# Kernel optimization log

Measured on AMD Instinct MI355X. Metric: run time of the kernel, lower is better.

Reference implementation:

```python
import jax, jax.numpy as jnp
import numpy as np

# Config (matches init_kwargs)
N, P, K, DIMS = 16, 1024, 16, 3
C_IN, C_MID, C_OUT, DM = 64, 64, 128, 4
C_CAT = C_MID + C_IN          # channels entering depthwise-separable conv
KK = K * K
BN_EPS = 1e-5


def setup_inputs() -> dict:
    key = jax.random.key(0)
    ks = jax.random.split(key, 24)
    s = 0.05  # small init scale for weights
    inp = {
        # forward args
        "rep_pt": jax.random.normal(ks[0], (N, P, DIMS), jnp.float32),
        "pts":    jax.random.normal(ks[1], (N, P, K, DIMS), jnp.float32),
        "fts":    jax.random.normal(ks[2], (N, P, K, C_IN), jnp.float32),
        # dense1 / dense2 (point lifting MLP), weights stored (in, out)
        "w1": jax.random.normal(ks[3], (DIMS, C_MID), jnp.float32) * s,
        "b1": jnp.zeros((C_MID,), jnp.float32),
        "w2": jax.random.normal(ks[4], (C_MID, C_MID), jnp.float32) * s,
        "b2": jnp.zeros((C_MID,), jnp.float32),
        # conv1: Conv2d(dims, K*K, (1,K)); weight (KK, dims, K)
        "wc1": jax.random.normal(ks[5], (KK, DIMS, K), jnp.float32) * s,
        "bc1": jnp.zeros((KK,), jnp.float32),
        # x_dense1 (ELU) and x_dense2 (no activation)
        "wx1": jax.random.normal(ks[6], (KK, KK), jnp.float32) * s,
        "bx1": jnp.zeros((KK,), jnp.float32),
        "wx2": jax.random.normal(ks[7], (KK, KK), jnp.float32) * s,
        "bx2": jnp.zeros((KK,), jnp.float32),
        # depthwise Conv2d(C_CAT, C_CAT*DM, (1,K), groups=C_CAT): weight (C_CAT, DM, K)
        "wdw": jax.random.normal(ks[8], (C_CAT, DM, K), jnp.float32) * s,
        "bdw": jnp.zeros((C_CAT * DM,), jnp.float32),
        # pointwise Conv2d(C_CAT*DM, C_OUT, 1): weight stored (C_CAT*DM, C_OUT)
        "wpw": jax.random.normal(ks[9], (C_CAT * DM, C_OUT), jnp.float32) * s,
        "bpw": jnp.zeros((C_OUT,), jnp.float32),
        # BatchNorm2d(C_OUT) in eval mode (running stats)
        "bn_gamma": jnp.ones((C_OUT,), jnp.float32),
        "bn_beta":  jnp.zeros((C_OUT,), jnp.float32),
        "bn_mean":  jax.random.normal(ks[10], (C_OUT,), jnp.float32) * 0.1,
        "bn_var":   jax.random.uniform(ks[11], (C_OUT,), jnp.float32, 0.5, 1.5),
    }
    return inp


def reference(rep_pt, pts, fts, w1, b1, w2, b2, wc1, bc1, wx1, bx1, wx2, bx2,
              wdw, bdw, wpw, bpw, bn_gamma, bn_beta, bn_mean, bn_var):
    elu = jax.nn.elu
    n, p, k = pts.shape[0], pts.shape[1], pts.shape[2]

    # localize points around representative point: (N,P,K,dims)
    pts_local = pts - rep_pt[:, :, None, :]

    # lift coordinates to C_mid features (two Dense+ELU)
    h = elu(pts_local @ w1 + b1)
    h = elu(h @ w2 + b2)
    fts_cat = jnp.concatenate([h, fts], axis=-1)  # (N,P,K,C_CAT)

    # learned X-transform: conv1 over the K neighbors -> (N,P,K*K)
    X = elu(jnp.einsum('npkd,odk->npo', pts_local, wc1) + bc1)
    X = elu(X @ wx1 + bx1)
    X = X @ wx2 + bx2            # x_dense2: no activation
    X = X.reshape(n, p, k, k)    # (N,P,K,K)

    # apply X-transform to concatenated features
    fts_X = jnp.einsum('npij,npjc->npic', X, fts_cat)  # (N,P,K,C_CAT)

    # depthwise conv (kernel (1,K), groups=C_CAT, depth multiplier DM)
    # torch grouped-conv channel order: out channel o = c*DM + d
    dw = jnp.einsum('npkc,cdk->npcd', fts_X, wdw).reshape(n, p, -1) + bdw
    # pointwise 1x1 conv -> C_OUT, then ELU
    y = elu(dw @ wpw + bpw)      # (N,P,C_OUT)
    # BatchNorm2d in eval mode (per-channel affine with running stats)
    y = (y - bn_mean) * (bn_gamma / jnp.sqrt(bn_var + BN_EPS)) + bn_beta
    return y                     # (N,P,C_OUT)
```

## Files before the change

kernel.cpp:

```cpp
#include <hip/hip_runtime.h>

#define NPTS 16384
#define MPB  16
#define NTHR 256
#define WS_NEEDED 401408u

typedef __attribute__((ext_vector_type(8))) short bf16x8;
typedef __attribute__((ext_vector_type(4))) float f32x4;

__device__ __forceinline__ unsigned short f2bf(float x) {
    unsigned u = __float_as_uint(x);
    return (unsigned short)((u + 0x7FFFu + ((u >> 16) & 1u)) >> 16);
}
__device__ __forceinline__ float bf2f(unsigned short h) {
    return __uint_as_float(((unsigned)h) << 16);
}
__device__ __forceinline__ float elu_f(float x) {
    return x > 0.f ? x : (__expf(x) - 1.f);
}

__device__ __forceinline__ bf16x8 load_bfrag(const float* __restrict__ W, int N,
                                             int kt, int nt, int lane) {
    int k0  = kt * 32 + ((lane >> 4) << 3);
    int col = nt * 16 + (lane & 15);
    const float* s = W + k0 * N + col;
    bf16x8 r;
#pragma unroll
    for (int j = 0; j < 8; j++) r[j] = (short)f2bf(s[j * N]);
    return r;
}

__global__ void pack_weights(const float* __restrict__ w2,
                             const float* __restrict__ wx1,
                             const float* __restrict__ wx2,
                             const float* __restrict__ wpw,
                             unsigned short* __restrict__ dst) {
    int gid  = blockIdx.x * 256 + threadIdx.x;
    int frag = gid >> 6, lane = gid & 63;
    const float* src; int N, fl;
    if      (frag <   8) { src = w2;  N =  64; fl = frag;       }
    else if (frag < 136) { src = wx1; N = 256; fl = frag - 8;   }
    else if (frag < 264) { src = wx2; N = 256; fl = frag - 136; }
    else                 { src = wpw; N = 128; fl = frag - 264; }
    int NT  = N >> 4;
    int kt  = fl / NT, nt = fl - kt * NT;
    int k0  = kt * 32 + (lane >> 4) * 8;
    int col = nt * 16 + (lane & 15);
    const float* s = src + k0 * N + col;
    unsigned v[4];
#pragma unroll
    for (int u = 0; u < 4; u++) {
        unsigned lo = f2bf(s[(2 * u) * N]);
        unsigned hi = f2bf(s[(2 * u + 1) * N]);
        v[u] = lo | (hi << 16);
    }
    *(uint4*)&dst[gid * 8] = make_uint4(v[0], v[1], v[2], v[3]);
}

template <bool PACKED>
__global__ __launch_bounds__(NTHR, 2)
void xconv_main(const float* __restrict__ rep_pt, const float* __restrict__ pts,
                const float* __restrict__ fts,
                const float* __restrict__ w1,  const float* __restrict__ b1,
                const float* __restrict__ w2,  const float* __restrict__ b2,
                const float* __restrict__ wc1, const float* __restrict__ bc1,
                const float* __restrict__ wx1, const float* __restrict__ bx1,
                const float* __restrict__ wx2, const float* __restrict__ bx2,
                const float* __restrict__ wdw, const float* __restrict__ bdw,
                const float* __restrict__ wpw, const float* __restrict__ bpw,
                const float* __restrict__ bn_gamma, const float* __restrict__ bn_beta,
                const float* __restrict__ bn_mean,  const float* __restrict__ bn_var,
                const unsigned short* __restrict__ wpack,
                float* __restrict__ out) {
    __shared__ __align__(16) char smem[62720];
    float*          s_ptsl = (float*)smem;
    unsigned short* s_h2   = (unsigned short*)(smem + 3072);
    unsigned short* s_h1   = (unsigned short*)(smem + 35840);
    unsigned short* s_x0   = (unsigned short*)(smem + 35840);
    unsigned short* s_x1   = (unsigned short*)(smem + 44288);
    unsigned short* s_dw   = (unsigned short*)(smem + 35840);
    unsigned short* s_x2   = (unsigned short*)(smem + 54272);

    const int t    = threadIdx.x;
    const int lane = t & 63;
    const int w    = t >> 6;
    const int gp0  = blockIdx.x * MPB;

    for (int idx = t; idx < MPB * 48; idx += NTHR) {
        int m = idx / 48, r = idx - m * 48;
        int k = r / 3,    d = r - k * 3;
        int gp = gp0 + m;
        s_ptsl[idx] = pts[(gp * 16 + k) * 3 + d] - rep_pt[gp * 3 + d];
    }
    __syncthreads();

    for (int R = 0; R < 2; R++) {
        {
            int lr  = t >> 1;
            int row = 128 * R + lr;
            int m = row >> 4, k = row & 15;
            float p0 = s_ptsl[m * 48 + k * 3 + 0];
            float p1 = s_ptsl[m * 48 + k * 3 + 1];
            float p2 = s_ptsl[m * 48 + k * 3 + 2];
            int cb = (t & 1) * 32;
#pragma unroll
            for (int cc = 0; cc < 4; cc++) {
                unsigned v[4];
#pragma unroll
                for (int u = 0; u < 4; u++) {
                    int c0 = cb + cc * 8 + u * 2;
                    float a  = fmaf(p0, w1[c0],       fmaf(p1, w1[64 + c0],     fmaf(p2, w1[128 + c0],     b1[c0])));
                    float bb = fmaf(p0, w1[c0 + 1],   fmaf(p1, w1[64 + c0 + 1], fmaf(p2, w1[128 + c0 + 1], b1[c0 + 1])));
                    v[u] = (unsigned)f2bf(elu_f(a)) | ((unsigned)f2bf(elu_f(bb)) << 16);
                }
                *(uint4*)&s_h1[lr * 72 + cb + cc * 8] = make_uint4(v[0], v[1], v[2], v[3]);
            }
        }
        __syncthreads();
        {
            const bf16x8* wp = (const bf16x8*)wpack;
            bf16x8 Bf[8];
#pragma unroll
            for (int f = 0; f < 8; f++) {
                if (PACKED) Bf[f] = wp[f * 64 + lane];
                else        Bf[f] = load_bfrag(w2, 64, f >> 2, f & 3, lane);
            }
            float bias[4];
#pragma unroll
            for (int nt = 0; nt < 4; nt++) bias[nt] = b2[nt * 16 + (lane & 15)];
#pragma unroll
            for (int i = 0; i < 2; i++) {
                int rtl = w * 2 + i;
                int g0  = (8 * R + rtl) * 16;
                bf16x8 a0 = *(const bf16x8*)&s_h1[(rtl * 16 + (lane & 15)) * 72 + 0  + (lane >> 4) * 8];
                bf16x8 a1 = *(const bf16x8*)&s_h1[(rtl * 16 + (lane & 15)) * 72 + 32 + (lane >> 4) * 8];
#pragma unroll
                for (int nt = 0; nt < 4; nt++) {
                    f32x4 acc = {bias[nt], bias[nt], bias[nt], bias[nt]};
                    acc = __builtin_amdgcn_mfma_f32_16x16x32_bf16(a0, Bf[0 * 4 + nt], acc, 0, 0, 0);
                    acc = __builtin_amdgcn_mfma_f32_16x16x32_bf16(a1, Bf[1 * 4 + nt], acc, 0, 0, 0);
#pragma unroll
                    for (int r = 0; r < 4; r++) {
                        int krow = (lane >> 4) * 4 + r;
                        s_h2[(g0 + krow) * 64 + nt * 16 + (lane & 15)] = f2bf(elu_f(acc[r]));
                    }
                }
            }
        }
        __syncthreads();
    }

    {
        float wreg[48];
#pragma unroll
        for (int q = 0; q < 12; q++) {
            float4 wv = *(const float4*)&wc1[t * 48 + q * 4];
            wreg[q * 4 + 0] = wv.x; wreg[q * 4 + 1] = wv.y;
            wreg[q * 4 + 2] = wv.z; wreg[q * 4 + 3] = wv.w;
        }
        float bo = bc1[t];
#pragma unroll 1
        for (int m = 0; m < MPB; m++) {
            float acc = bo;
#pragma unroll
            for (int q = 0; q < 12; q++) {
                float4 pv = *(const float4*)&s_ptsl[m * 48 + q * 4];
                acc = fmaf(pv.x, wreg[((q * 4 + 0) % 3) * 16 + (q * 4 + 0) / 3], acc);
                acc = fmaf(pv.y, wreg[((q * 4 + 1) % 3) * 16 + (q * 4 + 1) / 3], acc);
                acc = fmaf(pv.z, wreg[((q * 4 + 2) % 3) * 16 + (q * 4 + 2) / 3], acc);
                acc = fmaf(pv.w, wreg[((q * 4 + 3) % 3) * 16 + (q * 4 + 3) / 3], acc);
            }
            s_x0[m * 264 + t] = f2bf(elu_f(acc));
        }
    }
    __syncthreads();

    {
        const bf16x8* wp = (const bf16x8*)wpack + 512;
        f32x4 acc[4];
#pragma unroll
        for (int q = 0; q < 4; q++) {
            float bv = bx1[(w * 4 + q) * 16 + (lane & 15)];
            acc[q] = (f32x4){bv, bv, bv, bv};
        }
#pragma unroll
        for (int kt = 0; kt < 8; kt++) {
            bf16x8 a = *(const bf16x8*)&s_x0[(lane & 15) * 264 + kt * 32 + (lane >> 4) * 8];
#pragma unroll
            for (int q = 0; q < 4; q++) {
                int nt = w * 4 + q;
                bf16x8 b;
                if (PACKED) b = wp[(kt * 16 + nt) * 64 + lane];
                else        b = load_bfrag(wx1, 256, kt, nt, lane);
                acc[q] = __builtin_amdgcn_mfma_f32_16x16x32_bf16(a, b, acc[q], 0, 0, 0);
            }
        }
#pragma unroll
        for (int q = 0; q < 4; q++) {
            int nt = w * 4 + q;
#pragma unroll
            for (int r = 0; r < 4; r++) {
                int m = (lane >> 4) * 4 + r;
                s_x1[m * 264 + nt * 16 + (lane & 15)] = f2bf(elu_f(acc[q][r]));
            }
        }
    }
    __syncthreads();

    {
        const bf16x8* wp = (const bf16x8*)wpack + 8704;
        f32x4 acc[4];
#pragma unroll
        for (int q = 0; q < 4; q++) {
            float bv = bx2[(w * 4 + q) * 16 + (lane & 15)];
            acc[q] = (f32x4){bv, bv, bv, bv};
        }
#pragma unroll
        for (int kt = 0; kt < 8; kt++) {
            bf16x8 a = *(const bf16x8*)&s_x1[(lane & 15) * 264 + kt * 32 + (lane >> 4) * 8];
#pragma unroll
            for (int q = 0; q < 4; q++) {
                int nt = w * 4 + q;
                bf16x8 b;
                if (PACKED) b = wp[(kt * 16 + nt) * 64 + lane];
                else        b = load_bfrag(wx2, 256, kt, nt, lane);
                acc[q] = __builtin_amdgcn_mfma_f32_16x16x32_bf16(a, b, acc[q], 0, 0, 0);
            }
        }
#pragma unroll
        for (int q = 0; q < 4; q++) {
            int nt = w * 4 + q;
#pragma unroll
            for (int r = 0; r < 4; r++) {
                int m = (lane >> 4) * 4 + r;
                s_x2[m * 264 + nt * 16 + (lane & 15)] = f2bf(acc[q][r]);
            }
        }
    }
    __syncthreads();

    {
        const int c  = t & 127;
        const int mg = t >> 7;
        float wd[64];
#pragma unroll
        for (int q = 0; q < 16; q++) {
            float4 v = *(const float4*)&wdw[c * 64 + q * 4];
            wd[q * 4 + 0] = v.x; wd[q * 4 + 1] = v.y;
            wd[q * 4 + 2] = v.z; wd[q * 4 + 3] = v.w;
        }
        float bd[4];
#pragma unroll
        for (int d = 0; d < 4; d++) bd[d] = bdw[c * 4 + d];
#pragma unroll 1
        for (int ml = 0; ml < 8; ml++) {
            int m  = mg * 8 + ml;
            int gp = gp0 + m;
            float fc[16];
            if (c < 64) {
#pragma unroll
                for (int j = 0; j < 16; j++) fc[j] = bf2f(s_h2[(m * 16 + j) * 64 + c]);
            } else {
#pragma unroll
                for (int j = 0; j < 16; j++) fc[j] = fts[(gp * 16 + j) * 64 + (c - 64)];
            }
            float fXr[16];
#pragma unroll
            for (int i = 0; i < 16; i++) {
                float a = 0.f;
#pragma unroll
                for (int jj = 0; jj < 2; jj++) {
                    uint4 xv = *(const uint4*)&s_x2[m * 264 + i * 16 + jj * 8];
                    a = fmaf(__uint_as_float(xv.x << 16),          fc[jj * 8 + 0], a);
                    a = fmaf(__uint_as_float(xv.x & 0xFFFF0000u),  fc[jj * 8 + 1], a);
                    a = fmaf(__uint_as_float(xv.y << 16),          fc[jj * 8 + 2], a);
                    a = fmaf(__uint_as_float(xv.y & 0xFFFF0000u),  fc[jj * 8 + 3], a);
                    a = fmaf(__uint_as_float(xv.z << 16),          fc[jj * 8 + 4], a);
                    a = fmaf(__uint_as_float(xv.z & 0xFFFF0000u),  fc[jj * 8 + 5], a);
                    a = fmaf(__uint_as_float(xv.w << 16),          fc[jj * 8 + 6], a);
                    a = fmaf(__uint_as_float(xv.w & 0xFFFF0000u),  fc[jj * 8 + 7], a);
                }
                fXr[i] = a;
            }
            ushort4 dv;
            {
                float o[4];
#pragma unroll
                for (int d = 0; d < 4; d++) {
                    float a = bd[d];
#pragma unroll
                    for (int k = 0; k < 16; k++) a = fmaf(fXr[k], wd[d * 16 + k], a);
                    o[d] = a;
                }
                dv.x = f2bf(o[0]); dv.y = f2bf(o[1]); dv.z = f2bf(o[2]); dv.w = f2bf(o[3]);
            }
            *(ushort4*)&s_dw[m * 520 + c * 4] = dv;
        }
    }
    __syncthreads();

    {
        const bf16x8* wp = (const bf16x8*)wpack + 16896;
        f32x4 acc[2];
#pragma unroll
        for (int q = 0; q < 2; q++) {
            float bv = bpw[(w * 2 + q) * 16 + (lane & 15)];
            acc[q] = (f32x4){bv, bv, bv, bv};
        }
#pragma unroll
        for (int kt = 0; kt < 16; kt++) {
            bf16x8 a = *(const bf16x8*)&s_dw[(lane & 15) * 520 + kt * 32 + (lane >> 4) * 8];
#pragma unroll
            for (int q = 0; q < 2; q++) {
                int nt = w * 2 + q;
                bf16x8 b;
                if (PACKED) b = wp[(kt * 8 + nt) * 64 + lane];
                else        b = load_bfrag(wpw, 128, kt, nt, lane);
                acc[q] = __builtin_amdgcn_mfma_f32_16x16x32_bf16(a, b, acc[q], 0, 0, 0);
            }
        }
#pragma unroll
        for (int q = 0; q < 2; q++) {
            int co = (w * 2 + q) * 16 + (lane & 15);
            float scale = bn_gamma[co] * rsqrtf(bn_var[co] + 1e-5f);
            float shift = bn_beta[co] - bn_mean[co] * scale;
#pragma unroll
            for (int r = 0; r < 4; r++) {
                int m = (lane >> 4) * 4 + r;
                out[(gp0 + m) * 128 + co] = fmaf(elu_f(acc[q][r]), scale, shift);
            }
        }
    }
}

extern "C" void kernel_launch(void* const* d_in, const int* in_sizes, int n_in,
                              void* d_out, int out_size, void* d_ws, size_t ws_size,
                              hipStream_t stream) {
    const float* rep_pt   = (const float*)d_in[0];
    const float* pts      = (const float*)d_in[1];
    const float* fts      = (const float*)d_in[2];
    const float* w1       = (const float*)d_in[3];
    const float* b1       = (const float*)d_in[4];
    const float* w2       = (const float*)d_in[5];
    const float* b2       = (const float*)d_in[6];
    const float* wc1      = (const float*)d_in[7];
    const float* bc1      = (const float*)d_in[8];
    const float* wx1      = (const float*)d_in[9];
    const float* bx1      = (const float*)d_in[10];
    const float* wx2      = (const float*)d_in[11];
    const float* bx2      = (const float*)d_in[12];
    const float* wdw      = (const float*)d_in[13];
    const float* bdw      = (const float*)d_in[14];
    const float* wpw      = (const float*)d_in[15];
    const float* bpw      = (const float*)d_in[16];
    const float* bn_gamma = (const float*)d_in[17];
    const float* bn_beta  = (const float*)d_in[18];
    const float* bn_mean  = (const float*)d_in[19];
    const float* bn_var   = (const float*)d_in[20];
    float* out = (float*)d_out;

    const bool packed = (d_ws != nullptr) && (ws_size >= (size_t)WS_NEEDED);
    unsigned short* wpack = (unsigned short*)d_ws;

    if (packed) {
        pack_weights<<<98, 256, 0, stream>>>(w2, wx1, wx2, wpw, wpack);
        xconv_main<true><<<NPTS / MPB, NTHR, 0, stream>>>(
            rep_pt, pts, fts, w1, b1, w2, b2, wc1, bc1, wx1, bx1, wx2, bx2,
            wdw, bdw, wpw, bpw, bn_gamma, bn_beta, bn_mean, bn_var, wpack, out);
    } else {
        xconv_main<false><<<NPTS / MPB, NTHR, 0, stream>>>(
            rep_pt, pts, fts, w1, b1, w2, b2, wc1, bc1, wx1, bx1, wx2, bx2,
            wdw, bdw, wpw, bpw, bn_gamma, bn_beta, bn_mean, bn_var, (const unsigned short*)nullptr, out);
    }
}
```

Measured before the change: 204.2 us.

## Compute X-transform feature product with MFMA using fragment-packed LDS layouts

The per-point X·fts_cat product moves from scalar FMA loops onto 16x16x32 bf16 MFMA instructions. h2 and X2 are now written to shared memory already in MFMA fragment order, and the depthwise conv is reduced across lanes with shuffles. The w2 fragment loads are hoisted out of the R loop, and the fts loads are software-prefetched one point ahead. Half the lanes supply zero operands (K=16 padded to 32), and fts is now rounded to bf16, which reduces precision.

New measurement: 198.7 us. 1.03x faster.

```diff
diff --git a/kernel.cpp b/kernel.cpp
--- a/kernel.cpp
+++ b/kernel.cpp
@@ -11,6 +11,9 @@
 __device__ __forceinline__ unsigned short f2bf(float x) {
     unsigned u = __float_as_uint(x);
     return (unsigned short)((u + 0x7FFFu + ((u >> 16) & 1u)) >> 16);
+}
+__device__ __forceinline__ unsigned pk2(float a, float b) {
+    return (unsigned)f2bf(a) | ((unsigned)f2bf(b) << 16);
 }
 __device__ __forceinline__ float bf2f(unsigned short h) {
     return __uint_as_float(((unsigned)h) << 16);
@@ -72,18 +75,20 @@
                 const float* __restrict__ bn_mean,  const float* __restrict__ bn_var,
                 const unsigned short* __restrict__ wpack,
                 float* __restrict__ out) {
-    __shared__ __align__(16) char smem[62720];
+    __shared__ __align__(16) char smem[60928];
     float*          s_ptsl = (float*)smem;
-    unsigned short* s_h2   = (unsigned short*)(smem + 3072);
+    unsigned short* s_h2f  = (unsigned short*)(smem + 3072);
     unsigned short* s_h1   = (unsigned short*)(smem + 35840);
     unsigned short* s_x0   = (unsigned short*)(smem + 35840);
+    unsigned short* s_x2f  = (unsigned short*)(smem + 35840);
     unsigned short* s_x1   = (unsigned short*)(smem + 44288);
-    unsigned short* s_dw   = (unsigned short*)(smem + 35840);
-    unsigned short* s_x2   = (unsigned short*)(smem + 54272);
+    unsigned short* s_dw   = (unsigned short*)(smem + 44288);
 
     const int t    = threadIdx.x;
     const int lane = t & 63;
     const int w    = t >> 6;
+    const int cl   = lane & 15;
+    const int hh   = lane >> 4;
     const int gp0  = blockIdx.x * MPB;
 
     for (int idx = t; idx < MPB * 48; idx += NTHR) {
@@ -94,60 +99,62 @@
     }
     __syncthreads();
 
-    for (int R = 0; R < 2; R++) {
-        {
-            int lr  = t >> 1;
-            int row = 128 * R + lr;
-            int m = row >> 4, k = row & 15;
-            float p0 = s_ptsl[m * 48 + k * 3 + 0];
-            float p1 = s_ptsl[m * 48 + k * 3 + 1];
-            float p2 = s_ptsl[m * 48 + k * 3 + 2];
-            int cb = (t & 1) * 32;
-#pragma unroll
-            for (int cc = 0; cc < 4; cc++) {
-                unsigned v[4];
-#pragma unroll
-                for (int u = 0; u < 4; u++) {
-                    int c0 = cb + cc * 8 + u * 2;
-                    float a  = fmaf(p0, w1[c0],       fmaf(p1, w1[64 + c0],     fmaf(p2, w1[128 + c0],     b1[c0])));
-                    float bb = fmaf(p0, w1[c0 + 1],   fmaf(p1, w1[64 + c0 + 1], fmaf(p2, w1[128 + c0 + 1], b1[c0 + 1])));
-                    v[u] = (unsigned)f2bf(elu_f(a)) | ((unsigned)f2bf(elu_f(bb)) << 16);
+    {
+        const bf16x8* wp = (const bf16x8*)wpack;
+        bf16x8 Bf[8];
+#pragma unroll
+        for (int f = 0; f < 8; f++) {
+            if (PACKED) Bf[f] = wp[f * 64 + lane];
+            else        Bf[f] = load_bfrag(w2, 64, f >> 2, f & 3, lane);
+        }
+        float bias[4];
+#pragma unroll
+        for (int nt = 0; nt < 4; nt++) bias[nt] = b2[nt * 16 + cl];
+
+        for (int R = 0; R < 2; R++) {
+            {
+                int lr  = t >> 1;
+                int row = 128 * R + lr;
+                int m = row >> 4, k = row & 15;
+                float p0 = s_ptsl[m * 48 + k * 3 + 0];
+                float p1 = s_ptsl[m * 48 + k * 3 + 1];
+                float p2 = s_ptsl[m * 48 + k * 3 + 2];
+                int cb = (t & 1) * 32;
+#pragma unroll
+                for (int cc = 0; cc < 4; cc++) {
+                    unsigned v[4];
+#pragma unroll
+                    for (int u = 0; u < 4; u++) {
+                        int c0 = cb + cc * 8 + u * 2;
+                        float a  = fmaf(p0, w1[c0],     fmaf(p1, w1[64 + c0],     fmaf(p2, w1[128 + c0],     b1[c0])));
+                        float bb = fmaf(p0, w1[c0 + 1], fmaf(p1, w1[64 + c0 + 1], fmaf(p2, w1[128 + c0 + 1], b1[c0 + 1])));
+                        v[u] = pk2(elu_f(a), elu_f(bb));
+                    }
+                    *(uint4*)&s_h1[lr * 72 + cb + cc * 8] = make_uint4(v[0], v[1], v[2], v[3]);
                 }
-                *(uint4*)&s_h1[lr * 72 + cb + cc * 8] = make_uint4(v[0], v[1], v[2], v[3]);
-            }
-        }
-        __syncthreads();
-        {
-            const bf16x8* wp = (const bf16x8*)wpack;
-            bf16x8 Bf[8];
-#pragma unroll
-            for (int f = 0; f < 8; f++) {
-                if (PACKED) Bf[f] = wp[f * 64 + lane];
-                else        Bf[f] = load_bfrag(w2, 64, f >> 2, f & 3, lane);
-            }
-            float bias[4];
-#pragma unroll
-            for (int nt = 0; nt < 4; nt++) bias[nt] = b2[nt * 16 + (lane & 15)];
-#pragma unroll
-            for (int i = 0; i < 2; i++) {
-                int rtl = w * 2 + i;
-                int g0  = (8 * R + rtl) * 16;
-                bf16x8 a0 = *(const bf16x8*)&s_h1[(rtl * 16 + (lane & 15)) * 72 + 0  + (lane >> 4) * 8];
-                bf16x8 a1 = *(const bf16x8*)&s_h1[(rtl * 16 + (lane & 15)) * 72 + 32 + (lane >> 4) * 8];
-#pragma unroll
-                for (int nt = 0; nt < 4; nt++) {
-                    f32x4 acc = {bias[nt], bias[nt], bias[nt], bias[nt]};
-                    acc = __builtin_amdgcn_mfma_f32_16x16x32_bf16(a0, Bf[0 * 4 + nt], acc, 0, 0, 0);
-                    acc = __builtin_amdgcn_mfma_f32_16x16x32_bf16(a1, Bf[1 * 4 + nt], acc, 0, 0, 0);
-#pragma unroll
-                    for (int r = 0; r < 4; r++) {
-                        int krow = (lane >> 4) * 4 + r;
-                        s_h2[(g0 + krow) * 64 + nt * 16 + (lane & 15)] = f2bf(elu_f(acc[r]));
+            }
+            __syncthreads();
+            {
+#pragma unroll
+                for (int i = 0; i < 2; i++) {
+                    int rtl = w * 2 + i;
+                    int m   = 8 * R + rtl;
+                    bf16x8 a0 = *(const bf16x8*)&s_h1[(rtl * 16 + cl) * 72 + 0  + hh * 8];
+                    bf16x8 a1 = *(const bf16x8*)&s_h1[(rtl * 16 + cl) * 72 + 32 + hh * 8];
+#pragma unroll
+                    for (int nt = 0; nt < 4; nt++) {
+                        f32x4 acc = {bias[nt], bias[nt], bias[nt], bias[nt]};
+                        acc = __builtin_amdgcn_mfma_f32_16x16x32_bf16(a0, Bf[0 * 4 + nt], acc, 0, 0, 0);
+                        acc = __builtin_amdgcn_mfma_f32_16x16x32_bf16(a1, Bf[1 * 4 + nt], acc, 0, 0, 0);
+                        unsigned lo = pk2(elu_f(acc[0]), elu_f(acc[1]));
+                        unsigned hi = pk2(elu_f(acc[2]), elu_f(acc[3]));
+                        unsigned short* dp = &s_h2f[(((m * 4 + nt) * 32) + (hh >> 1) * 16 + cl) * 8 + (hh & 1) * 4];
+                        *(uint2*)dp = make_uint2(lo, hi);
                     }
                 }
             }
-        }
-        __syncthreads();
+            __syncthreads();
+        }
     }
 
     {
@@ -180,12 +187,12 @@
         f32x4 acc[4];
 #pragma unroll
         for (int q = 0; q < 4; q++) {
-            float bv = bx1[(w * 4 + q) * 16 + (lane & 15)];
+            float bv = bx1[(w * 4 + q) * 16 + cl];
             acc[q] = (f32x4){bv, bv, bv, bv};
         }
 #pragma unroll
         for (int kt = 0; kt < 8; kt++) {
-            bf16x8 a = *(const bf16x8*)&s_x0[(lane & 15) * 264 + kt * 32 + (lane >> 4) * 8];
+            bf16x8 a = *(const bf16x8*)&s_x0[cl * 264 + kt * 32 + hh * 8];
 #pragma unroll
             for (int q = 0; q < 4; q++) {
                 int nt = w * 4 + q;
@@ -200,8 +207,8 @@
             int nt = w * 4 + q;
 #pragma unroll
             for (int r = 0; r < 4; r++) {
-                int m = (lane >> 4) * 4 + r;
-                s_x1[m * 264 + nt * 16 + (lane & 15)] = f2bf(elu_f(acc[q][r]));
+                int m = hh * 4 + r;
+                s_x1[m * 264 + nt * 16 + cl] = f2bf(elu_f(acc[q][r]));
             }
         }
     }
@@ -212,12 +219,12 @@
         f32x4 acc[4];
 #pragma unroll
         for (int q = 0; q < 4; q++) {
-            float bv = bx2[(w * 4 + q) * 16 + (lane & 15)];
+            float bv = bx2[(w * 4 + q) * 16 + cl];
             acc[q] = (f32x4){bv, bv, bv, bv};
         }
 #pragma unroll
         for (int kt = 0; kt < 8; kt++) {
-            bf16x8 a = *(const bf16x8*)&s_x1[(lane & 15) * 264 + kt * 32 + (lane >> 4) * 8];
+            bf16x8 a = *(const bf16x8*)&s_x1[cl * 264 + kt * 32 + hh * 8];
 #pragma unroll
             for (int q = 0; q < 4; q++) {
                 int nt = w * 4 + q;
@@ -229,72 +236,93 @@
         }
 #pragma unroll
         for (int q = 0; q < 4; q++) {
-            int nt = w * 4 + q;
+            int ntE = w * 4 + q;
+            int lp  = (cl >> 3) * 16 + ntE;
+            int jj  = cl & 7;
 #pragma unroll
             for (int r = 0; r < 4; r++) {
-                int m = (lane >> 4) * 4 + r;
-                s_x2[m * 264 + nt * 16 + (lane & 15)] = f2bf(acc[q][r]);
+                int m = hh * 4 + r;
+                s_x2f[(m * 32 + lp) * 8 + jj] = f2bf(acc[q][r]);
             }
         }
     }
     __syncthreads();
 
     {
-        const int c  = t & 127;
-        const int mg = t >> 7;
-        float wd[64];
-#pragma unroll
-        for (int q = 0; q < 16; q++) {
-            float4 v = *(const float4*)&wdw[c * 64 + q * 4];
-            wd[q * 4 + 0] = v.x; wd[q * 4 + 1] = v.y;
-            wd[q * 4 + 2] = v.z; wd[q * 4 + 3] = v.w;
-        }
-        float bd[4];
-#pragma unroll
-        for (int d = 0; d < 4; d++) bd[d] = bdw[c * 4 + d];
-#pragma unroll 1
-        for (int ml = 0; ml < 8; ml++) {
-            int m  = mg * 8 + ml;
-            int gp = gp0 + m;
-            float fc[16];
-            if (c < 64) {
-#pragma unroll
-                for (int j = 0; j < 16; j++) fc[j] = bf2f(s_h2[(m * 16 + j) * 64 + c]);
-            } else {
-#pragma unroll
-                for (int j = 0; j < 16; j++) fc[j] = fts[(gp * 16 + j) * 64 + (c - 64)];
-            }
-            float fXr[16];
-#pragma unroll
-            for (int i = 0; i < 16; i++) {
-                float a = 0.f;
-#pragma unroll
-                for (int jj = 0; jj < 2; jj++) {
-                    uint4 xv = *(const uint4*)&s_x2[m * 264 + i * 16 + jj * 8];
-                    a = fmaf(__uint_as_float(xv.x << 16),          fc[jj * 8 + 0], a);
-                    a = fmaf(__uint_as_float(xv.x & 0xFFFF0000u),  fc[jj * 8 + 1], a);
-                    a = fmaf(__uint_as_float(xv.y << 16),          fc[jj * 8 + 2], a);
-                    a = fmaf(__uint_as_float(xv.y & 0xFFFF0000u),  fc[jj * 8 + 3], a);
-                    a = fmaf(__uint_as_float(xv.z << 16),          fc[jj * 8 + 4], a);
-                    a = fmaf(__uint_as_float(xv.z & 0xFFFF0000u),  fc[jj * 8 + 5], a);
-                    a = fmaf(__uint_as_float(xv.w << 16),          fc[jj * 8 + 6], a);
-                    a = fmaf(__uint_as_float(xv.w & 0xFFFF0000u),  fc[jj * 8 + 7], a);
-                }
-                fXr[i] = a;
-            }
-            ushort4 dv;
-            {
-                float o[4];
-#pragma unroll
-                for (int d = 0; d < 4; d++) {
-                    float a = bd[d];
-#pragma unroll
-                    for (int k = 0; k < 16; k++) a = fmaf(fXr[k], wd[d * 16 + k], a);
-                    o[d] = a;
-                }
-                dv.x = f2bf(o[0]); dv.y = f2bf(o[1]); dv.z = f2bf(o[2]); dv.w = f2bf(o[3]);
-            }
-            *(ushort4*)&s_dw[m * 520 + c * 4] = dv;
+        const int cA = w * 16 + cl;
+        const int cB = 64 + w * 16 + cl;
+        float wdA[16], wdB[16];
+#pragma unroll
+        for (int d = 0; d < 4; d++) {
+            float4 va = *(const float4*)&wdw[cA * 64 + d * 16 + 4 * hh];
+            wdA[d * 4 + 0] = va.x; wdA[d * 4 + 1] = va.y; wdA[d * 4 + 2] = va.z; wdA[d * 4 + 3] = va.w;
+            float4 vb = *(const float4*)&wdw[cB * 64 + d * 16 + 4 * hh];
+            wdB[d * 4 + 0] = vb.x; wdB[d * 4 + 1] = vb.y; wdB[d * 4 + 2] = vb.z; wdB[d * 4 + 3] = vb.w;
+        }
+        float4 bdA = *(const float4*)&bdw[cA * 4];
+        float4 bdB = *(const float4*)&bdw[cB * 4];
+        const float* ftsp = fts + (size_t)gp0 * 1024 + (w * 16 + cl);
+
+        float f0[8], f1[8];
+        auto LDF = [&](int m, float* f) {
+            if (lane < 32) {
+                const float* p = ftsp + (m * 16 + hh * 8) * 64;
+#pragma unroll
+                for (int j = 0; j < 8; j++) f[j] = p[j * 64];
+            }
+        };
+        auto BODY = [&](int m, float* fc_, float* fn_) {
+            if (m < 15) LDF(m + 1, fn_);
+            bf16x8 a  = {};
+            bf16x8 bh = {};
+            if (lane < 32) {
+                a  = *(const bf16x8*)&s_x2f[(m * 32 + lane) * 8];
+                bh = *(const bf16x8*)&s_h2f[((m * 4 + w) * 32 + lane) * 8];
+            }
+            f32x4 accA = {0.f, 0.f, 0.f, 0.f};
+            f32x4 accB = {0.f, 0.f, 0.f, 0.f};
+            accA = __builtin_amdgcn_mfma_f32_16x16x32_bf16(a, bh, accA, 0, 0, 0);
+            bf16x8 bf_ = {};
+            if (lane < 32) {
+                union { bf16x8 v; uint4 u; } ub;
+                ub.u = make_uint4(pk2(fc_[0], fc_[1]), pk2(fc_[2], fc_[3]),
+                                  pk2(fc_[4], fc_[5]), pk2(fc_[6], fc_[7]));
+                bf_ = ub.v;
+            }
+            accB = __builtin_amdgcn_mfma_f32_16x16x32_bf16(a, bf_, accB, 0, 0, 0);
+            float oA[4], oB[4];
+#pragma unroll
+            for (int d = 0; d < 4; d++) {
+                float sA = accA[0] * wdA[d * 4 + 0];
+                sA = fmaf(accA[1], wdA[d * 4 + 1], sA);
+                sA = fmaf(accA[2], wdA[d * 4 + 2], sA);
+                sA = fmaf(accA[3], wdA[d * 4 + 3], sA);
+                sA += __shfl_xor(sA, 16);
+                sA += __shfl_xor(sA, 32);
+                oA[d] = sA;
+                float sB = accB[0] * wdB[d * 4 + 0];
+                sB = fmaf(accB[1], wdB[d * 4 + 1], sB);
+                sB = fmaf(accB[2], wdB[d * 4 + 2], sB);
+                sB = fmaf(accB[3], wdB[d * 4 + 3], sB);
+                sB += __shfl_xor(sB, 16);
+                sB += __shfl_xor(sB, 32);
+                oB[d] = sB;
+            }
+            if (hh == 0) {
+                ushort4 va, vb;
+                va.x = f2bf(oA[0] + bdA.x); va.y = f2bf(oA[1] + bdA.y);
+                va.z = f2bf(oA[2] + bdA.z); va.w = f2bf(oA[3] + bdA.w);
+                vb.x = f2bf(oB[0] + bdB.x); vb.y = f2bf(oB[1] + bdB.y);
+                vb.z = f2bf(oB[2] + bdB.z); vb.w = f2bf(oB[3] + bdB.w);
+                *(ushort4*)&s_dw[m * 520 + cA * 4] = va;
+                *(ushort4*)&s_dw[m * 520 + cB * 4] = vb;
+            }
+        };
+        LDF(0, f0);
+#pragma unroll
+        for (int mm = 0; mm < 8; mm++) {
+            BODY(2 * mm + 0, f0, f1);
+            BODY(2 * mm + 1, f1, f0);
         }
     }
     __syncthreads();
@@ -304,12 +332,12 @@
         f32x4 acc[2];
 #pragma unroll
         for (int q = 0; q < 2; q++) {
-            float bv = bpw[(w * 2 + q) * 16 + (lane & 15)];
+            float bv = bpw[(w * 2 + q) * 16 + cl];
             acc[q] = (f32x4){bv, bv, bv, bv};
         }
 #pragma unroll
         for (int kt = 0; kt < 16; kt++) {
-            bf16x8 a = *(const bf16x8*)&s_dw[(lane & 15) * 520 + kt * 32 + (lane >> 4) * 8];
+            bf16x8 a = *(const bf16x8*)&s_dw[cl * 520 + kt * 32 + hh * 8];
 #pragma unroll
             for (int q = 0; q < 2; q++) {
                 int nt = w * 2 + q;
@@ -321,12 +349,12 @@
         }
 #pragma unroll
         for (int q = 0; q < 2; q++) {
-            int co = (w * 2 + q) * 16 + (lane & 15);
+            int co = (w * 2 + q) * 16 + cl;
             float scale = bn_gamma[co] * rsqrtf(bn_var[co] + 1e-5f);
             float shift = bn_beta[co] - bn_mean[co] * scale;
 #pragma unroll
             for (int r = 0; r < 4; r++) {
-                int m = (lane >> 4) * 4 + r;
+                int m = hh * 4 + r;
                 out[(gp0 + m) * 128 + co] = fmaf(elu_f(acc[q][r]), scale, shift);
             }
         }
```
